# Optimization experiments

Measured on AMD Instinct MI355X. Metric: run time of the kernel, lower is better.

Reference implementation:

```python
import jax, jax.numpy as jnp
import numpy as np

B, N, C, H = 8, 1024, 768, 12
D = C // H  # head_dim = 64
SCALE = D ** -0.5
EPS = 1e-5  # nn.LayerNorm default


def layer_norm(x, gamma, beta):
    # normalize over last dim (head_dim)
    mu = jnp.mean(x, axis=-1, keepdims=True)
    var = jnp.var(x, axis=-1, keepdims=True)
    return (x - mu) * jax.lax.rsqrt(var + EPS) * gamma + beta


def setup_inputs() -> dict:
    key = jax.random.key(0)
    ks = jax.random.split(key, 5)
    s = 0.02
    return {
        "x": jax.random.normal(ks[0], (B, N, C), jnp.float32),
        "qkv_w": jax.random.normal(ks[1], (3 * C, C), jnp.float32) * s,
        "qkv_b": jax.random.normal(ks[2], (3 * C,), jnp.float32) * s,
        "q_gamma": jnp.ones((D,), jnp.float32),
        "q_beta": jnp.zeros((D,), jnp.float32),
        "k_gamma": jnp.ones((D,), jnp.float32),
        "k_beta": jnp.zeros((D,), jnp.float32),
        "proj_w": jax.random.normal(ks[3], (C, C), jnp.float32) * s,
        "proj_b": jax.random.normal(ks[4], (C,), jnp.float32) * s,
    }


def reference(x, qkv_w, qkv_b, q_gamma, q_beta, k_gamma, k_beta, proj_w, proj_b):
    Bx, Nx, Cx = x.shape
    qkv = x @ qkv_w.T + qkv_b                       # [B,N,3C]
    qkv = qkv.reshape(Bx, Nx, 3, H, D).transpose(2, 0, 3, 1, 4)  # [3,B,H,N,D]
    q, k, v = qkv[0], qkv[1], qkv[2]
    q = layer_norm(q, q_gamma, q_beta) * SCALE
    k = layer_norm(k, k_gamma, k_beta)
    attn = jax.nn.softmax(jnp.einsum('bhnd,bhmd->bhnm', q, k), axis=-1)  # [B,H,N,N]
    # attn_drop is identity (p=0, eval)
    out = jnp.einsum('bhnm,bhmd->bhnd', attn, v)    # [B,H,N,D]
    out = out.transpose(0, 2, 1, 3).reshape(Bx, Nx, Cx)
    out = out @ proj_w.T + proj_b                   # proj_drop identity
    return out, attn
```

## Files before the change

kernel.cpp:

```cpp
#include <hip/hip_runtime.h>
#include <hip/hip_bf16.h>
#include <stdint.h>

typedef __bf16 bf16_t;
typedef __bf16 bf16x8 __attribute__((ext_vector_type(8)));
typedef float f32x4 __attribute__((ext_vector_type(4)));

#define DEV static __device__ __forceinline__

DEV f32x4 mfma16(bf16x8 a, bf16x8 b, f32x4 c) {
  return __builtin_amdgcn_mfma_f32_16x16x32_bf16(a, b, c, 0, 0, 0);
}

DEV void gll16(const void* g, void* l) {
  __builtin_amdgcn_global_load_lds(
      (const __attribute__((address_space(1))) uint32_t*)g,
      (__attribute__((address_space(3))) uint32_t*)l, 16, 0, 0);
}

DEV int swz128(int row, int c16) {
  return (row << 7) + (((c16 ^ row) & 7) << 4);
}
DEV int swzel128(int row, int col) {
  return (row << 7) + ((((col >> 3) ^ row) & 7) << 4) + ((col & 7) << 1);
}

DEV void stage_tile_gll(const bf16_t* g, long rstride, char* lds, int wave, int lane) {
  int r0 = wave * 8 + (lane >> 3);
  int b = lane & 7;
#pragma unroll
  for (int q = 0; q < 2; q++) {
    int row = q * 32 + r0;
    gll16(g + (long)row * rstride + (((b ^ row) & 7) << 3),
          lds + q * 4096 + wave * 1024);
  }
}

__global__ void __launch_bounds__(256)
cast_all(const float* __restrict__ x, bf16_t* __restrict__ ox,
         const float* __restrict__ w1, bf16_t* __restrict__ ow1,
         const float* __restrict__ w2, bf16_t* __restrict__ ow2) {
  long i = (long)(blockIdx.x * 256 + threadIdx.x) * 8;
  const float* s; bf16_t* d; long off;
  if (i < 6291456L)      { s = x;  d = ox;  off = i; }
  else if (i < 8060928L) { s = w1; d = ow1; off = i - 6291456L; }
  else if (i < 8650752L) { s = w2; d = ow2; off = i - 8060928L; }
  else return;
  float4 a = *(const float4*)(s + off);
  float4 b = *(const float4*)(s + off + 4);
  bf16x8 v;
  v[0] = (bf16_t)a.x; v[1] = (bf16_t)a.y; v[2] = (bf16_t)a.z; v[3] = (bf16_t)a.w;
  v[4] = (bf16_t)b.x; v[5] = (bf16_t)b.y; v[6] = (bf16_t)b.z; v[7] = (bf16_t)b.w;
  *(bf16x8*)(d + off) = v;
}

#define C1Q 0.1803368801111244f

__global__ void __launch_bounds__(256, 2)
gemm_qkv_ln(const bf16_t* __restrict__ A, const bf16_t* __restrict__ Bw,
            const float* __restrict__ bias,
            const float* __restrict__ qg, const float* __restrict__ qb,
            const float* __restrict__ kg, const float* __restrict__ kb,
            bf16_t* __restrict__ qkv, int M, int N, int K) {
  __shared__ __align__(16) char As[8192];
  __shared__ __align__(16) char Bs[8192];
  const int tid = threadIdx.x;
  const int lane = tid & 63;
  const int wave = tid >> 6;
  const int wr = wave >> 1, wc = wave & 1;
  const int tileM = blockIdx.y << 7;
  const int tileN = blockIdx.x << 7;
  const int lrow = lane & 15, lk = lane >> 4;

  f32x4 acc[4][4];
  f32x4 z = {0.f, 0.f, 0.f, 0.f};
#pragma unroll
  for (int m = 0; m < 4; m++)
#pragma unroll
    for (int n = 0; n < 4; n++) acc[m][n] = z;

  const int srow = wave * 16 + (lane >> 2);
  const int sb = lane & 3;
  const bf16_t* Asrc0 = A + (long)(tileM + srow) * K + sb * 8;
  const bf16_t* Asrc1 = A + (long)(tileM + 64 + srow) * K + sb * 8;
  const bf16_t* Bsrc0 = Bw + (long)(tileN + srow) * K + sb * 8;
  const bf16_t* Bsrc1 = Bw + (long)(tileN + 64 + srow) * K + sb * 8;
  char* Adst = As + wave * 1024;
  char* Bdst = Bs + wave * 1024;

  for (int k0 = 0; k0 < K; k0 += 32) {
    __syncthreads();
    gll16(Asrc0 + k0, Adst);
    gll16(Asrc1 + k0, Adst + 4096);
    gll16(Bsrc0 + k0, Bdst);
    gll16(Bsrc1 + k0, Bdst + 4096);
    __syncthreads();
    bf16x8 af[4], bfr[4];
#pragma unroll
    for (int m = 0; m < 4; m++)
      af[m] = *(const bf16x8*)(As + (wr * 64 + m * 16 + lrow) * 64 + lk * 16);
#pragma unroll
    for (int n = 0; n < 4; n++)
      bfr[n] = *(const bf16x8*)(Bs + (wc * 64 + n * 16 + lrow) * 64 + lk * 16);
#pragma unroll
    for (int m = 0; m < 4; m++)
#pragma unroll
      for (int n = 0; n < 4; n++)
        acc[m][n] = mfma16(af[m], bfr[n], acc[m][n]);
  }

  const int t = tileN / 768;
  const int cbase = tileN + wc * 64;
  float g[4], be[4], bv[4];
#pragma unroll
  for (int n = 0; n < 4; n++) bv[n] = bias[cbase + n * 16 + lrow];
  if (t == 0) {
#pragma unroll
    for (int n = 0; n < 4; n++) {
      int d = n * 16 + lrow;
      g[n] = qg[d] * C1Q; be[n] = qb[d] * C1Q;
    }
  } else if (t == 1) {
#pragma unroll
    for (int n = 0; n < 4; n++) {
      int d = n * 16 + lrow;
      g[n] = kg[d]; be[n] = kb[d];
    }
  }

#pragma unroll
  for (int m = 0; m < 4; m++) {
#pragma unroll
    for (int r = 0; r < 4; r++) {
      float v[4];
#pragma unroll
      for (int n = 0; n < 4; n++) v[n] = acc[m][n][r] + bv[n];
      long row = tileM + wr * 64 + m * 16 + lk * 4 + r;
      bf16_t* dst = qkv + row * 2304 + cbase;
      if (t < 2) {
        float s = v[0] + v[1] + v[2] + v[3];
        float s2 = v[0]*v[0] + v[1]*v[1] + v[2]*v[2] + v[3]*v[3];
#pragma unroll
        for (int ofs = 1; ofs <= 8; ofs <<= 1) {
          s  += __shfl_xor(s, ofs);
          s2 += __shfl_xor(s2, ofs);
        }
        float mu = s * (1.f / 64.f);
        float rstd = rsqrtf(s2 * (1.f / 64.f) - mu * mu + 1e-5f);
#pragma unroll
        for (int n = 0; n < 4; n++)
          dst[n * 16 + lrow] = (bf16_t)((v[n] - mu) * rstd * g[n] + be[n]);
      } else {
#pragma unroll
        for (int n = 0; n < 4; n++)
          dst[n * 16 + lrow] = (bf16_t)v[n];
      }
    }
  }
}

__global__ void __launch_bounds__(256, 2)
gemm_bt(const bf16_t* __restrict__ A, const bf16_t* __restrict__ Bw,
        const float* __restrict__ bias, float* __restrict__ Cout,
        int M, int N, int K) {
  __shared__ __align__(16) char As[8192];
  __shared__ __align__(16) char Bs[8192];
  const int tid = threadIdx.x;
  const int lane = tid & 63;
  const int wave = tid >> 6;
  const int wr = wave >> 1, wc = wave & 1;
  const int tileM = blockIdx.y << 7;
  const int tileN = blockIdx.x << 7;
  const int lrow = lane & 15, lk = lane >> 4;

  f32x4 acc[4][4];
  f32x4 z = {0.f, 0.f, 0.f, 0.f};
#pragma unroll
  for (int m = 0; m < 4; m++)
#pragma unroll
    for (int n = 0; n < 4; n++) acc[m][n] = z;

  const int srow = wave * 16 + (lane >> 2);
  const int sb = lane & 3;
  const bf16_t* Asrc0 = A + (long)(tileM + srow) * K + sb * 8;
  const bf16_t* Asrc1 = A + (long)(tileM + 64 + srow) * K + sb * 8;
  const bf16_t* Bsrc0 = Bw + (long)(tileN + srow) * K + sb * 8;
  const bf16_t* Bsrc1 = Bw + (long)(tileN + 64 + srow) * K + sb * 8;
  char* Adst = As + wave * 1024;
  char* Bdst = Bs + wave * 1024;

  for (int k0 = 0; k0 < K; k0 += 32) {
    __syncthreads();
    gll16(Asrc0 + k0, Adst);
    gll16(Asrc1 + k0, Adst + 4096);
    gll16(Bsrc0 + k0, Bdst);
    gll16(Bsrc1 + k0, Bdst + 4096);
    __syncthreads();
    bf16x8 af[4], bfr[4];
#pragma unroll
    for (int m = 0; m < 4; m++)
      af[m] = *(const bf16x8*)(As + (wr * 64 + m * 16 + lrow) * 64 + lk * 16);
#pragma unroll
    for (int n = 0; n < 4; n++)
      bfr[n] = *(const bf16x8*)(Bs + (wc * 64 + n * 16 + lrow) * 64 + lk * 16);
#pragma unroll
    for (int m = 0; m < 4; m++)
#pragma unroll
      for (int n = 0; n < 4; n++)
        acc[m][n] = mfma16(af[m], bfr[n], acc[m][n]);
  }

  const int rg = lk;
#pragma unroll
  for (int n = 0; n < 4; n++) {
    int col = tileN + wc * 64 + n * 16 + lrow;
    float bv = bias[col];
#pragma unroll
    for (int m = 0; m < 4; m++) {
      long row0 = tileM + wr * 64 + m * 16 + rg * 4;
#pragma unroll
      for (int r = 0; r < 4; r++)
        Cout[(row0 + r) * N + col] = acc[m][n][r] + bv;
    }
  }
}

__global__ void __launch_bounds__(256, 2)
attn_kernel(const bf16_t* __restrict__ qkv, float* __restrict__ attn_out,
            bf16_t* __restrict__ out_heads) {
  const int tid = threadIdx.x;
  const int lane = tid & 63;
  const int wave = tid >> 6;
  const int qt = blockIdx.x;
  const int bh = blockIdx.y;
  const int b = bh / 12, h = bh - b * 12;

  const bf16_t* base = qkv + (long)b * 2359296L + h * 64;
  const bf16_t* Qg = base;
  const bf16_t* Kg = base + 768;
  const bf16_t* Vg = base + 1536;

  __shared__ __align__(16) char Ks[16384];
  __shared__ __align__(16) char Vt[8192];
  __shared__ __align__(16) char QP[8192];
  __shared__ __align__(16) float ATs[64 * 68];

  const int lrow = lane & 15;
  const int lk = lane >> 4;

  stage_tile_gll(Qg + (long)(qt * 64) * 2304, 2304, QP, wave, lane);
  stage_tile_gll(Kg, 2304, Ks, wave, lane);
  __syncthreads();

  bf16x8 qf[2];
  qf[0] = *(const bf16x8*)(QP + swz128(wave * 16 + lrow, lk));
  qf[1] = *(const bf16x8*)(QP + swz128(wave * 16 + lrow, 4 + lk));

  auto computeS = [&](const char* Kb, f32x4 sfr[4]) {
    f32x4 z = {0.f, 0.f, 0.f, 0.f};
    sfr[0] = z; sfr[1] = z; sfr[2] = z; sfr[3] = z;
#pragma unroll
    for (int kk = 0; kk < 2; kk++)
#pragma unroll
      for (int f = 0; f < 4; f++) {
        bf16x8 kf = *(const bf16x8*)(Kb + swz128(f * 16 + lrow, kk * 4 + lk));
        sfr[f] = mfma16(qf[kk], kf, sfr[f]);
      }
  };

  float l_r[4] = {0.f, 0.f, 0.f, 0.f};

  for (int kt = 0; kt < 16; kt++) {
    if (kt < 15)
      stage_tile_gll(Kg + (long)((kt + 1) * 64) * 2304, 2304,
                     Ks + ((kt + 1) & 1) * 8192, wave, lane);
    f32x4 sfr[4];
    computeS(Ks + (kt & 1) * 8192, sfr);
#pragma unroll
    for (int r = 0; r < 4; r++)
      l_r[r] += exp2f(sfr[0][r]) + exp2f(sfr[1][r]) +
                exp2f(sfr[2][r]) + exp2f(sfr[3][r]);
    __syncthreads();
  }

  float il[4];
#pragma unroll
  for (int r = 0; r < 4; r++) {
#pragma unroll
    for (int ofs = 1; ofs <= 8; ofs <<= 1)
      l_r[r] += __shfl_xor(l_r[r], ofs);
    il[r] = 1.0f / l_r[r];
  }

  f32x4 of[4];
  {
    f32x4 z = {0.f, 0.f, 0.f, 0.f};
    of[0] = z; of[1] = z; of[2] = z; of[3] = z;
  }
  char* Pw = QP + wave * 2048;
  float* attn_base = attn_out + (long)bh * 1048576;

  stage_tile_gll(Kg, 2304, Ks, wave, lane);
  const int vk = lane;
  const int vdg = wave;
  bf16x8 vr0 = *(const bf16x8*)(Vg + (long)vk * 2304 + vdg * 16);
  bf16x8 vr1 = *(const bf16x8*)(Vg + (long)vk * 2304 + vdg * 16 + 8);

  for (int kt = 0; kt < 16; kt++) {
    __syncthreads();
#pragma unroll
    for (int j = 0; j < 8; j++) {
      *(bf16_t*)(Vt + swzel128(vdg * 16 + j, vk)) = vr0[j];
      *(bf16_t*)(Vt + swzel128(vdg * 16 + 8 + j, vk)) = vr1[j];
    }
    f32x4 sfr[4];
    computeS(Ks + (kt & 1) * 8192, sfr);
#pragma unroll
    for (int f = 0; f < 4; f++)
#pragma unroll
      for (int r = 0; r < 4; r++) {
        float p = exp2f(sfr[f][r]) * il[r];
        int lr = lk * 4 + r;
        int col = f * 16 + lrow;
        ATs[(wave * 16 + lr) * 68 + col] = p;
        *(bf16_t*)(Pw + swzel128(lr, col)) = (bf16_t)p;
      }
    __syncthreads();
    if (kt < 15) {
      stage_tile_gll(Kg + (long)((kt + 1) * 64) * 2304, 2304,
                     Ks + ((kt + 1) & 1) * 8192, wave, lane);
      const bf16_t* vp = Vg + (long)((kt + 1) * 64 + vk) * 2304 + vdg * 16;
      vr0 = *(const bf16x8*)(vp);
      vr1 = *(const bf16x8*)(vp + 8);
    }
#pragma unroll
    for (int kk = 0; kk < 2; kk++) {
      bf16x8 pf = *(const bf16x8*)(Pw + swz128(lrow, kk * 4 + lk));
#pragma unroll
      for (int f = 0; f < 4; f++) {
        bf16x8 vf = *(const bf16x8*)(Vt + swz128(f * 16 + lrow, kk * 4 + lk));
        of[f] = mfma16(pf, vf, of[f]);
      }
    }
    float* ab = attn_base + ((long)(qt * 64) << 10) + kt * 64;
#pragma unroll
    for (int i = 0; i < 4; i++) {
      int idx = i * 256 + tid;
      int row = idx >> 4, c4 = idx & 15;
      f32x4 v = *(const f32x4*)(ATs + row * 68 + c4 * 4);
      __builtin_nontemporal_store(v, (f32x4*)(ab + ((long)row << 10) + c4 * 4));
    }
  }

#pragma unroll
  for (int f = 0; f < 4; f++)
#pragma unroll
    for (int r = 0; r < 4; r++) {
      int nrow = qt * 64 + wave * 16 + lk * 4 + r;
      int d = f * 16 + lrow;
      out_heads[((long)b * 1024 + nrow) * 768 + h * 64 + d] = (bf16_t)of[f][r];
    }
}

extern "C" void kernel_launch(void* const* d_in, const int* in_sizes, int n_in,
                              void* d_out, int out_size, void* d_ws, size_t ws_size,
                              hipStream_t stream) {
  (void)in_sizes; (void)n_in; (void)out_size; (void)ws_size;
  const float* x       = (const float*)d_in[0];
  const float* qkv_w   = (const float*)d_in[1];
  const float* qkv_b   = (const float*)d_in[2];
  const float* q_gamma = (const float*)d_in[3];
  const float* q_beta  = (const float*)d_in[4];
  const float* k_gamma = (const float*)d_in[5];
  const float* k_beta  = (const float*)d_in[6];
  const float* proj_w  = (const float*)d_in[7];
  const float* proj_b  = (const float*)d_in[8];
  float* out = (float*)d_out;

  char* ws = (char*)d_ws;
  bf16_t* x_bf      = (bf16_t*)(ws);
  bf16_t* wqkv      = (bf16_t*)(ws + 12582912L);
  bf16_t* wproj     = (bf16_t*)(ws + 16121856L);
  bf16_t* qkv       = (bf16_t*)(ws + 17301504L);
  bf16_t* out_heads = (bf16_t*)(ws + 55050240L);

  cast_all<<<4224, 256, 0, stream>>>(x, x_bf, qkv_w, wqkv, proj_w, wproj);
  gemm_qkv_ln<<<dim3(18, 64), 256, 0, stream>>>(x_bf, wqkv, qkv_b,
                                                q_gamma, q_beta, k_gamma, k_beta,
                                                qkv, 8192, 2304, 768);
  attn_kernel<<<dim3(16, 96), 256, 0, stream>>>(qkv, out + 6291456L, out_heads);
  gemm_bt<<<dim3(6, 64), 256, 0, stream>>>(out_heads, wproj, proj_b, out, 8192, 768, 768);
}
```

Before: 215.8 us.

## Process 128 query rows per attention block and write attn from bf16 LDS

Each attention block now covers 128 query rows instead of 64, so every K and V tile fetched from global memory feeds twice as many MFMAs, and the grid is halved. The fp32 ATs staging buffer is removed. The attention-probability output is instead read back from the bf16 P tile in LDS and widened to fp32 before the nontemporal store. This saves LDS (launch bounds raised to 3 blocks per CU) but rounds the returned attn matrix to bf16 precision, which may exceed tolerance.

```diff
diff --git a/kernel.cpp b/kernel.cpp
--- a/kernel.cpp
+++ b/kernel.cpp
@@ -225,7 +225,7 @@
   }
 }
 
-__global__ void __launch_bounds__(256, 2)
+__global__ void __launch_bounds__(256, 3)
 attn_kernel(const bf16_t* __restrict__ qkv, float* __restrict__ attn_out,
             bf16_t* __restrict__ out_heads) {
   const int tid = threadIdx.x;
@@ -242,67 +242,85 @@
 
   __shared__ __align__(16) char Ks[16384];
   __shared__ __align__(16) char Vt[8192];
-  __shared__ __align__(16) char QP[8192];
-  __shared__ __align__(16) float ATs[64 * 68];
+  __shared__ __align__(16) char QP[16384];
 
   const int lrow = lane & 15;
   const int lk = lane >> 4;
-
-  stage_tile_gll(Qg + (long)(qt * 64) * 2304, 2304, QP, wave, lane);
+  const int w32 = wave * 32;
+
+  stage_tile_gll(Qg + (long)(qt * 128) * 2304, 2304, QP, wave, lane);
+  stage_tile_gll(Qg + (long)(qt * 128 + 64) * 2304, 2304, QP + 8192, wave, lane);
   stage_tile_gll(Kg, 2304, Ks, wave, lane);
   __syncthreads();
 
-  bf16x8 qf[2];
-  qf[0] = *(const bf16x8*)(QP + swz128(wave * 16 + lrow, lk));
-  qf[1] = *(const bf16x8*)(QP + swz128(wave * 16 + lrow, 4 + lk));
-
-  auto computeS = [&](const char* Kb, f32x4 sfr[4]) {
+  bf16x8 qf[2][2];
+#pragma unroll
+  for (int rf = 0; rf < 2; rf++)
+#pragma unroll
+    for (int kk = 0; kk < 2; kk++)
+      qf[rf][kk] = *(const bf16x8*)(QP + swz128(w32 + rf * 16 + lrow, kk * 4 + lk));
+
+  auto computeS = [&](const char* Kb, f32x4 sfr[2][4]) {
     f32x4 z = {0.f, 0.f, 0.f, 0.f};
-    sfr[0] = z; sfr[1] = z; sfr[2] = z; sfr[3] = z;
-#pragma unroll
-    for (int kk = 0; kk < 2; kk++)
-#pragma unroll
-      for (int f = 0; f < 4; f++) {
-        bf16x8 kf = *(const bf16x8*)(Kb + swz128(f * 16 + lrow, kk * 4 + lk));
-        sfr[f] = mfma16(qf[kk], kf, sfr[f]);
-      }
+#pragma unroll
+    for (int rf = 0; rf < 2; rf++)
+#pragma unroll
+      for (int f = 0; f < 4; f++) sfr[rf][f] = z;
+#pragma unroll
+    for (int kk = 0; kk < 2; kk++) {
+      bf16x8 kf[4];
+#pragma unroll
+      for (int f = 0; f < 4; f++)
+        kf[f] = *(const bf16x8*)(Kb + swz128(f * 16 + lrow, kk * 4 + lk));
+#pragma unroll
+      for (int rf = 0; rf < 2; rf++)
+#pragma unroll
+        for (int f = 0; f < 4; f++)
+          sfr[rf][f] = mfma16(qf[rf][kk], kf[f], sfr[rf][f]);
+    }
   };
 
-  float l_r[4] = {0.f, 0.f, 0.f, 0.f};
+  float l_r[2][4] = {{0.f,0.f,0.f,0.f},{0.f,0.f,0.f,0.f}};
 
   for (int kt = 0; kt < 16; kt++) {
     if (kt < 15)
       stage_tile_gll(Kg + (long)((kt + 1) * 64) * 2304, 2304,
                      Ks + ((kt + 1) & 1) * 8192, wave, lane);
-    f32x4 sfr[4];
+    f32x4 sfr[2][4];
     computeS(Ks + (kt & 1) * 8192, sfr);
 #pragma unroll
-    for (int r = 0; r < 4; r++)
-      l_r[r] += exp2f(sfr[0][r]) + exp2f(sfr[1][r]) +
-                exp2f(sfr[2][r]) + exp2f(sfr[3][r]);
-    __syncthreads();
-  }
-
-  float il[4];
-#pragma unroll
-  for (int r = 0; r < 4; r++) {
-#pragma unroll
-    for (int ofs = 1; ofs <= 8; ofs <<= 1)
-      l_r[r] += __shfl_xor(l_r[r], ofs);
-    il[r] = 1.0f / l_r[r];
-  }
-
-  f32x4 of[4];
+    for (int rf = 0; rf < 2; rf++)
+#pragma unroll
+      for (int r = 0; r < 4; r++)
+        l_r[rf][r] += exp2f(sfr[rf][0][r]) + exp2f(sfr[rf][1][r]) +
+                      exp2f(sfr[rf][2][r]) + exp2f(sfr[rf][3][r]);
+    __syncthreads();
+  }
+
+  float il[2][4];
+#pragma unroll
+  for (int rf = 0; rf < 2; rf++)
+#pragma unroll
+    for (int r = 0; r < 4; r++) {
+      float l = l_r[rf][r];
+#pragma unroll
+      for (int ofs = 1; ofs <= 8; ofs <<= 1) l += __shfl_xor(l, ofs);
+      il[rf][r] = 1.0f / l;
+    }
+
+  f32x4 of[2][4];
   {
     f32x4 z = {0.f, 0.f, 0.f, 0.f};
-    of[0] = z; of[1] = z; of[2] = z; of[3] = z;
-  }
-  char* Pw = QP + wave * 2048;
-  float* attn_base = attn_out + (long)bh * 1048576;
+#pragma unroll
+    for (int rf = 0; rf < 2; rf++)
+#pragma unroll
+      for (int f = 0; f < 4; f++) of[rf][f] = z;
+  }
+  char* Plds = QP;
+  float* attn_base = attn_out + (long)bh * 1048576 + ((long)(qt * 128) << 10);
 
   stage_tile_gll(Kg, 2304, Ks, wave, lane);
-  const int vk = lane;
-  const int vdg = wave;
+  const int vk = lane, vdg = wave;
   bf16x8 vr0 = *(const bf16x8*)(Vg + (long)vk * 2304 + vdg * 16);
   bf16x8 vr1 = *(const bf16x8*)(Vg + (long)vk * 2304 + vdg * 16 + 8);
 
@@ -313,18 +331,19 @@
       *(bf16_t*)(Vt + swzel128(vdg * 16 + j, vk)) = vr0[j];
       *(bf16_t*)(Vt + swzel128(vdg * 16 + 8 + j, vk)) = vr1[j];
     }
-    f32x4 sfr[4];
+    f32x4 sfr[2][4];
     computeS(Ks + (kt & 1) * 8192, sfr);
 #pragma unroll
-    for (int f = 0; f < 4; f++)
-#pragma unroll
-      for (int r = 0; r < 4; r++) {
-        float p = exp2f(sfr[f][r]) * il[r];
-        int lr = lk * 4 + r;
-        int col = f * 16 + lrow;
-        ATs[(wave * 16 + lr) * 68 + col] = p;
-        *(bf16_t*)(Pw + swzel128(lr, col)) = (bf16_t)p;
-      }
+    for (int rf = 0; rf < 2; rf++)
+#pragma unroll
+      for (int f = 0; f < 4; f++)
+#pragma unroll
+        for (int r = 0; r < 4; r++) {
+          float p = exp2f(sfr[rf][f][r]) * il[rf][r];
+          int row = w32 + rf * 16 + lk * 4 + r;
+          int col = f * 16 + lrow;
+          *(bf16_t*)(Plds + swzel128(row, col)) = (bf16_t)p;
+        }
     __syncthreads();
     if (kt < 15) {
       stage_tile_gll(Kg + (long)((kt + 1) * 64) * 2304, 2304,
@@ -335,31 +354,42 @@
     }
 #pragma unroll
     for (int kk = 0; kk < 2; kk++) {
-      bf16x8 pf = *(const bf16x8*)(Pw + swz128(lrow, kk * 4 + lk));
+      bf16x8 pf[2];
+#pragma unroll
+      for (int rf = 0; rf < 2; rf++)
+        pf[rf] = *(const bf16x8*)(Plds + swz128(w32 + rf * 16 + lrow, kk * 4 + lk));
 #pragma unroll
       for (int f = 0; f < 4; f++) {
         bf16x8 vf = *(const bf16x8*)(Vt + swz128(f * 16 + lrow, kk * 4 + lk));
-        of[f] = mfma16(pf, vf, of[f]);
+#pragma unroll
+        for (int rf = 0; rf < 2; rf++)
+          of[rf][f] = mfma16(pf[rf], vf, of[rf][f]);
       }
     }
-    float* ab = attn_base + ((long)(qt * 64) << 10) + kt * 64;
+    float* ab = attn_base + kt * 64;
 #pragma unroll
     for (int i = 0; i < 4; i++) {
       int idx = i * 256 + tid;
-      int row = idx >> 4, c4 = idx & 15;
-      f32x4 v = *(const f32x4*)(ATs + row * 68 + c4 * 4);
-      __builtin_nontemporal_store(v, (f32x4*)(ab + ((long)row << 10) + c4 * 4));
-    }
-  }
-
-#pragma unroll
-  for (int f = 0; f < 4; f++)
-#pragma unroll
-    for (int r = 0; r < 4; r++) {
-      int nrow = qt * 64 + wave * 16 + lk * 4 + r;
-      int d = f * 16 + lrow;
-      out_heads[((long)b * 1024 + nrow) * 768 + h * 64 + d] = (bf16_t)of[f][r];
-    }
+      int row = idx >> 3, c16 = idx & 7;
+      bf16x8 pv = *(const bf16x8*)(Plds + swz128(row, c16));
+      f32x4 lo = {(float)pv[0], (float)pv[1], (float)pv[2], (float)pv[3]};
+      f32x4 hi = {(float)pv[4], (float)pv[5], (float)pv[6], (float)pv[7]};
+      float* dst = ab + ((long)row << 10) + c16 * 8;
+      __builtin_nontemporal_store(lo, (f32x4*)dst);
+      __builtin_nontemporal_store(hi, (f32x4*)(dst + 4));
+    }
+  }
+
+#pragma unroll
+  for (int rf = 0; rf < 2; rf++)
+#pragma unroll
+    for (int f = 0; f < 4; f++)
+#pragma unroll
+      for (int r = 0; r < 4; r++) {
+        int nrow = qt * 128 + w32 + rf * 16 + lk * 4 + r;
+        int d = f * 16 + lrow;
+        out_heads[((long)b * 1024 + nrow) * 768 + h * 64 + d] = (bf16_t)of[rf][f][r];
+      }
 }
 
 extern "C" void kernel_launch(void* const* d_in, const int* in_sizes, int n_in,
@@ -388,6 +418,6 @@
   gemm_qkv_ln<<<dim3(18, 64), 256, 0, stream>>>(x_bf, wqkv, qkv_b,
                                                 q_gamma, q_beta, k_gamma, k_beta,
                                                 qkv, 8192, 2304, 768);
-  attn_kernel<<<dim3(16, 96), 256, 0, stream>>>(qkv, out + 6291456L, out_heads);
+  attn_kernel<<<dim3(8, 96), 256, 0, stream>>>(qkv, out + 6291456L, out_heads);
   gemm_bt<<<dim3(6, 64), 256, 0, stream>>>(out_heads, wproj, proj_b, out, 8192, 768, 768);
 }
```

Result: slower. 359.2 us (+66.5%).
